# Performance work log

Measured on AMD Instinct MI355X. Metric: run time of the kernel, lower is better.

## Reference

```python
import jax, jax.numpy as jnp
import numpy as np

BS, SEQ, H, L = 2, 4096, 768, 8921

def setup_inputs() -> dict:
    key = jax.random.key(0)
    k1, k2, k3 = jax.random.split(key, 3)
    return {
        "code_features": jax.random.normal(k1, (L, H), dtype=jnp.float32),
        "text_features": jax.random.normal(k2, (BS, SEQ, H), dtype=jnp.float32),
        "attention_mask": jnp.ones((BS, SEQ), dtype=jnp.int32),
        "W": jax.random.normal(k3, (H, H), dtype=jnp.float32) * (1.0 / np.sqrt(H)),
    }

def reference(code_features, text_features, attention_mask, W):
    # projected = tanh(Linear(text)) : (bs, seq, h)
    projected = jnp.tanh(jnp.einsum("bsh,kh->bsk", text_features, W))
    # scores: (bs, seq, labels); code_features broadcasts over batch
    scores = jnp.einsum("bsh,lh->bsl", projected, code_features)
    # softmax over the SEQ axis (dim=1), then transpose -> (bs, labels, seq)
    att_weights = jnp.transpose(jax.nn.softmax(scores, axis=1), (0, 2, 1))
    # weighted sum over seq -> (bs, labels, h)
    weighted_output = jnp.einsum("bls,bsh->blh", att_weights, text_features)
    return (att_weights, weighted_output)
```

## Files before the change

### kernel.cpp

```cpp
#include <hip/hip_runtime.h>
#include <math.h>

#define BSZ  2
#define SEQN 4096
#define HD   768
#define NL   8921

typedef _Float16 f16;
typedef f16   f16x8 __attribute__((ext_vector_type(8)));
typedef float f32x4 __attribute__((ext_vector_type(4)));

#define GPTR(p) ((const __attribute__((address_space(1))) void*)(p))
#define LPTR(p) ((__attribute__((address_space(3))) void*)(p))

__device__ __forceinline__ void stage_region(const f16* __restrict__ src, int ldk,
                                             int row0, int rowMax, int kbase,
                                             f16* region, int t)
{
    const int lane = t & 63, wv = t >> 6;
    #pragma unroll
    for (int qq = 0; qq < 2; ++qq) {
        const int base16 = wv * 64 + qq * 512;
        const int off16  = base16 + lane;
        const int row    = off16 >> 2;
        const int chunk  = off16 & 3;
        const int schunk = chunk ^ ((row >> 1) & 3);
        int grow = row0 + row; if (grow > rowMax) grow = rowMax;
        const f16* g = src + (long long)grow * ldk + kbase + schunk * 8;
        __builtin_amdgcn_global_load_lds(GPTR(g), LPTR(region + base16 * 8), 16, 0, 0);
    }
}

#define PH_SYNC_ENTER()                                          \
    __builtin_amdgcn_sched_barrier(0);                           \
    __builtin_amdgcn_s_barrier();                                \
    asm volatile("s_waitcnt lgkmcnt(0)" ::: "memory");           \
    __builtin_amdgcn_sched_barrier(0);                           \
    __builtin_amdgcn_s_setprio(1);

#define PH_SYNC_EXIT()                                           \
    __builtin_amdgcn_s_setprio(0);                               \
    __builtin_amdgcn_sched_barrier(0);                           \
    __builtin_amdgcn_s_barrier();

template<int OUT>
__global__ __launch_bounds__(512, 2)
void gemm8p(const f16* __restrict__ A, const f16* __restrict__ B,
            void* __restrict__ C, int M, int N, int K,
            long long sA, long long sB, long long sC, int ldA, int ldB)
{
    __shared__ __align__(16) f16 SH[2][2][2][256 * 32];

    const int t    = threadIdx.x;
    const int lane = t & 63;
    const int wv   = t >> 6;
    const int wm   = wv >> 2;
    const int wn   = wv & 3;
    const int rl   = lane & 15;
    const int swz8 = (((lane >> 4) ^ ((rl >> 1) & 3)) * 8);

    const int nx = gridDim.x, nwg = nx * gridDim.y;
    int orig = blockIdx.y * nx + blockIdx.x;
    const int q = nwg >> 3, r = nwg & 7, xcd = orig & 7, sub = orig >> 3;
    const int wg = (xcd < r ? xcd * (q + 1) : r * (q + 1) + (xcd - r) * q) + sub;
    const int bx = wg % nx, by = wg / nx;

    const f16* Ab = A + (long long)blockIdx.z * sA;
    const f16* Bb = B + (long long)blockIdx.z * sB;

    const int m0 = by * 256, n0 = bx * 256;
    const int NT = K >> 6;
    const int Mm1 = M - 1, Nm1 = N - 1;

    f32x4 acc[8][4];
    #pragma unroll
    for (int i = 0; i < 8; ++i)
        #pragma unroll
        for (int j = 0; j < 4; ++j)
            acc[i][j] = (f32x4)0.f;

    stage_region(Ab, ldA, m0, Mm1, 0,  &SH[0][0][0][0], t);
    stage_region(Bb, ldB, n0, Nm1, 0,  &SH[0][1][0][0], t);
    stage_region(Ab, ldA, m0, Mm1, 32, &SH[0][0][1][0], t);
    stage_region(Bb, ldB, n0, Nm1, 32, &SH[0][1][1][0], t);
    stage_region(Ab, ldA, m0, Mm1, 64, &SH[1][0][0][0], t);
    stage_region(Bb, ldB, n0, Nm1, 64, &SH[1][1][0][0], t);
    stage_region(Ab, ldA, m0, Mm1, 96, &SH[1][0][1][0], t);
    asm volatile("s_waitcnt vmcnt(6)" ::: "memory");
    __builtin_amdgcn_sched_barrier(0);
    __builtin_amdgcn_s_barrier();

    for (int tt = 0; tt < NT; ++tt) {
        const int buf = tt & 1;
        const f16* As0 = &SH[buf][0][0][0];
        const f16* As1 = &SH[buf][0][1][0];
        const f16* Bs0 = &SH[buf][1][0][0];
        const f16* Bs1 = &SH[buf][1][1][0];

        f16x8 af[8], bfa, bfb, bfc, bfd;

        #pragma unroll
        for (int f = 0; f < 8; ++f)
            af[f] = *(const f16x8*)&As0[(wm * 128 + f * 16 + rl) * 32 + swz8];
        bfa = *(const f16x8*)&Bs0[(wn * 64 + 0 * 16 + rl) * 32 + swz8];
        bfb = *(const f16x8*)&Bs0[(wn * 64 + 1 * 16 + rl) * 32 + swz8];
        if (tt + 1 < NT)
            stage_region(Bb, ldB, n0, Nm1, (tt + 1) * 64 + 32, &SH[buf ^ 1][1][1][0], t);
        PH_SYNC_ENTER();
        #pragma unroll
        for (int f = 0; f < 8; ++f) {
            acc[f][0] = __builtin_amdgcn_mfma_f32_16x16x32_f16(af[f], bfa, acc[f][0], 0, 0, 0);
            acc[f][1] = __builtin_amdgcn_mfma_f32_16x16x32_f16(af[f], bfb, acc[f][1], 0, 0, 0);
        }
        PH_SYNC_EXIT();

        bfc = *(const f16x8*)&Bs0[(wn * 64 + 2 * 16 + rl) * 32 + swz8];
        bfd = *(const f16x8*)&Bs0[(wn * 64 + 3 * 16 + rl) * 32 + swz8];
        if (tt + 2 < NT)
            stage_region(Ab, ldA, m0, Mm1, (tt + 2) * 64, &SH[buf][0][0][0], t);
        PH_SYNC_ENTER();
        #pragma unroll
        for (int f = 0; f < 8; ++f) {
            acc[f][2] = __builtin_amdgcn_mfma_f32_16x16x32_f16(af[f], bfc, acc[f][2], 0, 0, 0);
            acc[f][3] = __builtin_amdgcn_mfma_f32_16x16x32_f16(af[f], bfd, acc[f][3], 0, 0, 0);
        }
        PH_SYNC_EXIT();

        #pragma unroll
        for (int f = 0; f < 8; ++f)
            af[f] = *(const f16x8*)&As1[(wm * 128 + f * 16 + rl) * 32 + swz8];
        bfa = *(const f16x8*)&Bs1[(wn * 64 + 0 * 16 + rl) * 32 + swz8];
        bfb = *(const f16x8*)&Bs1[(wn * 64 + 1 * 16 + rl) * 32 + swz8];
        if (tt + 2 < NT)
            stage_region(Bb, ldB, n0, Nm1, (tt + 2) * 64, &SH[buf][1][0][0], t);
        PH_SYNC_ENTER();
        #pragma unroll
        for (int f = 0; f < 8; ++f) {
            acc[f][0] = __builtin_amdgcn_mfma_f32_16x16x32_f16(af[f], bfa, acc[f][0], 0, 0, 0);
            acc[f][1] = __builtin_amdgcn_mfma_f32_16x16x32_f16(af[f], bfb, acc[f][1], 0, 0, 0);
        }
        PH_SYNC_EXIT();

        bfc = *(const f16x8*)&Bs1[(wn * 64 + 2 * 16 + rl) * 32 + swz8];
        bfd = *(const f16x8*)&Bs1[(wn * 64 + 3 * 16 + rl) * 32 + swz8];
        if (tt + 2 < NT)
            stage_region(Ab, ldA, m0, Mm1, (tt + 2) * 64 + 32, &SH[buf][0][1][0], t);
        __builtin_amdgcn_sched_barrier(0);
        __builtin_amdgcn_s_barrier();
        asm volatile("s_waitcnt lgkmcnt(0)" ::: "memory");
        __builtin_amdgcn_sched_barrier(0);
        __builtin_amdgcn_s_setprio(1);
        #pragma unroll
        for (int f = 0; f < 8; ++f) {
            acc[f][2] = __builtin_amdgcn_mfma_f32_16x16x32_f16(af[f], bfc, acc[f][2], 0, 0, 0);
            acc[f][3] = __builtin_amdgcn_mfma_f32_16x16x32_f16(af[f], bfd, acc[f][3], 0, 0, 0);
        }
        __builtin_amdgcn_s_setprio(0);
        asm volatile("s_waitcnt vmcnt(6)" ::: "memory");
        __builtin_amdgcn_sched_barrier(0);
        __builtin_amdgcn_s_barrier();
    }

    const int rq = (lane >> 4) * 4;
    #pragma unroll
    for (int f = 0; f < 8; ++f) {
        #pragma unroll
        for (int j = 0; j < 4; ++j) {
            #pragma unroll
            for (int rr = 0; rr < 4; ++rr) {
                const int row = m0 + wm * 128 + f * 16 + rq + rr;
                const int col = n0 + wn * 64 + j * 16 + rl;
                if (row < M) {
                    if constexpr (OUT == 1)
                        ((f16*)C + (long long)blockIdx.z * sC)[(long long)row * N + col] = (f16)acc[f][j][rr];
                    else
                        ((float*)C + (long long)blockIdx.z * sC)[(long long)row * N + col] = acc[f][j][rr];
                }
            }
        }
    }
}

template<int S16>
__device__ inline void stage_tile(const void* srcv, int ldk, int row0, int rowMax,
                                  int kt, f16* dst, int t, int lane, int wv)
{
    if constexpr (S16) {
        const f16* src = (const f16*)srcv;
        #pragma unroll
        for (int j = 0; j < 2; ++j) {
            int r = wv * 32 + j * 16 + (lane >> 2);
            int row = row0 + r; if (row > rowMax) row = rowMax;
            const f16* g = src + (long long)row * ldk + kt + (lane & 3) * 8;
            f16* l = dst + (wv * 32 + j * 16) * 32;
            __builtin_amdgcn_global_load_lds(GPTR(g), LPTR(l), 16, 0, 0);
        }
    } else {
        const float* src = (const float*)srcv;
        int r  = t >> 1;
        int kq = (t & 1) * 16;
        int row = row0 + r; if (row > rowMax) row = rowMax;
        const float* g = src + (long long)row * ldk + kt + kq;
        float4 v0 = ((const float4*)g)[0];
        float4 v1 = ((const float4*)g)[1];
        float4 v2 = ((const float4*)g)[2];
        float4 v3 = ((const float4*)g)[3];
        f16x8 h0, h1;
        h0[0]=(f16)v0.x; h0[1]=(f16)v0.y; h0[2]=(f16)v0.z; h0[3]=(f16)v0.w;
        h0[4]=(f16)v1.x; h0[5]=(f16)v1.y; h0[6]=(f16)v1.z; h0[7]=(f16)v1.w;
        h1[0]=(f16)v2.x; h1[1]=(f16)v2.y; h1[2]=(f16)v2.z; h1[3]=(f16)v2.w;
        h1[4]=(f16)v3.x; h1[5]=(f16)v3.y; h1[6]=(f16)v3.z; h1[7]=(f16)v3.w;
        *(f16x8*)&dst[r * 32 + kq]     = h0;
        *(f16x8*)&dst[r * 32 + kq + 8] = h1;
    }
}

template<int SA, int SB, int OUTMODE>
__global__ __launch_bounds__(256)
void mfma_nt(const void* __restrict__ A, const void* __restrict__ B,
             void* __restrict__ C, int M, int N, int K,
             long long sA, long long sB, long long sC, int ldA, int ldB)
{
    const char* Ab = (const char*)A + (long long)blockIdx.z * sA * (SA ? 2 : 4);
    const char* Bb = (const char*)B + (long long)blockIdx.z * sB * (SB ? 2 : 4);

    __shared__ __align__(16) f16 As[128 * 32];
    __shared__ __align__(16) f16 Bs[128 * 32];

    const int t    = threadIdx.x;
    const int lane = t & 63;
    const int wv   = t >> 6;
    const int wr   = wv >> 1;
    const int wc   = wv & 1;
    const int m0   = blockIdx.y * 128;
    const int n0   = blockIdx.x * 128;

    f32x4 acc[4][4] = {};

    for (int kt = 0; kt < K; kt += 32) {
        stage_tile<SA>(Ab, ldA, m0, M - 1, kt, As, t, lane, wv);
        stage_tile<SB>(Bb, ldB, n0, N - 1, kt, Bs, t, lane, wv);
        __syncthreads();

        f16x8 af[4], bf[4];
        const int kc = (lane >> 4) * 8;
        const int rl = lane & 15;
        #pragma unroll
        for (int i = 0; i < 4; ++i)
            af[i] = *(const f16x8*)&As[(wr * 64 + i * 16 + rl) * 32 + kc];
        #pragma unroll
        for (int j = 0; j < 4; ++j)
            bf[j] = *(const f16x8*)&Bs[(wc * 64 + j * 16 + rl) * 32 + kc];

        #pragma unroll
        for (int i = 0; i < 4; ++i)
            #pragma unroll
            for (int j = 0; j < 4; ++j)
                acc[i][j] = __builtin_amdgcn_mfma_f32_16x16x32_f16(af[i], bf[j], acc[i][j], 0, 0, 0);
        __syncthreads();
    }

    const int rquad = (lane >> 4) * 4;
    const int rcol  = lane & 15;
    #pragma unroll
    for (int i = 0; i < 4; ++i) {
        #pragma unroll
        for (int j = 0; j < 4; ++j) {
            #pragma unroll
            for (int r = 0; r < 4; ++r) {
                int row = m0 + wr * 64 + i * 16 + rquad + r;
                int col = n0 + wc * 64 + j * 16 + rcol;
                if (row < M) {
                    if constexpr (OUTMODE == 1)
                        ((f16*)C)[(long long)row * N + col] = (f16)tanhf(acc[i][j][r]);
                    else
                        ((float*)C + (long long)blockIdx.z * sC)[(long long)row * N + col] = acc[i][j][r];
                }
            }
        }
    }
}

__global__ __launch_bounds__(256)
void cvt_f32_f16(const float* __restrict__ in, f16* __restrict__ out, long long n4)
{
    long long i = (long long)blockIdx.x * 256 + threadIdx.x;
    if (i < n4) {
        float4 v = ((const float4*)in)[i];
        f16 h[4] = {(f16)v.x, (f16)v.y, (f16)v.z, (f16)v.w};
        *(uint2*)&out[i * 4] = *(uint2*)h;
    }
}

__global__ __launch_bounds__(256)
void transpose_f16(const float* __restrict__ in, f16* __restrict__ out)
{
    __shared__ float tile[32][33];
    const int b  = blockIdx.z;
    const int h0 = blockIdx.x * 32, s0 = blockIdx.y * 32;
    in  += (long long)b * SEQN * HD;
    out += (long long)b * HD * SEQN;
    const int tx = threadIdx.x & 31, ty = threadIdx.x >> 5;
    #pragma unroll
    for (int i = ty; i < 32; i += 8)
        tile[i][tx] = in[(long long)(s0 + i) * HD + h0 + tx];
    __syncthreads();
    #pragma unroll
    for (int i = ty; i < 32; i += 8)
        out[(long long)(h0 + i) * SEQN + s0 + tx] = (f16)tile[tx][i];
}

__global__ __launch_bounds__(256)
void softmax_f16(f16* __restrict__ scores, float* __restrict__ att)
{
    const long long row = blockIdx.x;
    f16*   ps = scores + row * (long long)SEQN;
    float* pa = att    + row * (long long)SEQN;
    const int t = threadIdx.x;

    f16x8 h[2];
    float x[2][8];
    float vmax = -INFINITY;
    #pragma unroll
    for (int i = 0; i < 2; ++i) {
        h[i] = ((const f16x8*)ps)[t + 256 * i];
        #pragma unroll
        for (int j = 0; j < 8; ++j) {
            x[i][j] = (float)h[i][j];
            vmax = fmaxf(vmax, x[i][j]);
        }
    }
    #pragma unroll
    for (int off = 32; off > 0; off >>= 1)
        vmax = fmaxf(vmax, __shfl_xor(vmax, off));

    __shared__ float redmax[4];
    __shared__ float redsum[4];
    if ((t & 63) == 0) redmax[t >> 6] = vmax;
    __syncthreads();
    vmax = fmaxf(fmaxf(redmax[0], redmax[1]), fmaxf(redmax[2], redmax[3]));

    float sum = 0.f;
    #pragma unroll
    for (int i = 0; i < 2; ++i)
        #pragma unroll
        for (int j = 0; j < 8; ++j) {
            x[i][j] = expf(x[i][j] - vmax);
            sum += x[i][j];
        }
    #pragma unroll
    for (int off = 32; off > 0; off >>= 1)
        sum += __shfl_xor(sum, off);
    if ((t & 63) == 0) redsum[t >> 6] = sum;
    __syncthreads();
    sum = (redsum[0] + redsum[1]) + (redsum[2] + redsum[3]);

    const float inv = 1.0f / sum;
    #pragma unroll
    for (int i = 0; i < 2; ++i) {
        f16x8 hn;
        #pragma unroll
        for (int j = 0; j < 8; ++j) {
            x[i][j] *= inv;
            hn[j] = (f16)x[i][j];
        }
        float4 lo = make_float4(x[i][0], x[i][1], x[i][2], x[i][3]);
        float4 hi = make_float4(x[i][4], x[i][5], x[i][6], x[i][7]);
        ((float4*)pa)[(t + 256 * i) * 2 + 0] = lo;
        ((float4*)pa)[(t + 256 * i) * 2 + 1] = hi;
        ((f16x8*)ps)[t + 256 * i] = hn;
    }
}

#define BMF 64
#define BNF 64
#define BKF 16
#define PADF 4

__global__ __launch_bounds__(256)
void softmax_rows_f32(float* __restrict__ data)
{
    const long long row = blockIdx.x;
    float* p = data + row * (long long)SEQN;
    const int t = threadIdx.x;
    float4 v[4];
    float vmax = -INFINITY;
    #pragma unroll
    for (int i = 0; i < 4; ++i) {
        v[i] = ((const float4*)p)[t + 256 * i];
        vmax = fmaxf(vmax, fmaxf(fmaxf(v[i].x, v[i].y), fmaxf(v[i].z, v[i].w)));
    }
    #pragma unroll
    for (int off = 32; off > 0; off >>= 1)
        vmax = fmaxf(vmax, __shfl_xor(vmax, off));
    __shared__ float redmax[4];
    __shared__ float redsum[4];
    if ((t & 63) == 0) redmax[t >> 6] = vmax;
    __syncthreads();
    vmax = fmaxf(fmaxf(redmax[0], redmax[1]), fmaxf(redmax[2], redmax[3]));
    float sum = 0.f;
    #pragma unroll
    for (int i = 0; i < 4; ++i) {
        v[i].x = expf(v[i].x - vmax); v[i].y = expf(v[i].y - vmax);
        v[i].z = expf(v[i].z - vmax); v[i].w = expf(v[i].w - vmax);
        sum += (v[i].x + v[i].y) + (v[i].z + v[i].w);
    }
    #pragma unroll
    for (int off = 32; off > 0; off >>= 1)
        sum += __shfl_xor(sum, off);
    if ((t & 63) == 0) redsum[t >> 6] = sum;
    __syncthreads();
    sum = (redsum[0] + redsum[1]) + (redsum[2] + redsum[3]);
    const float inv = 1.0f / sum;
    #pragma unroll
    for (int i = 0; i < 4; ++i) {
        v[i].x *= inv; v[i].y *= inv; v[i].z *= inv; v[i].w *= inv;
        ((float4*)p)[t + 256 * i] = v[i];
    }
}

template<bool TANH>
__global__ __launch_bounds__(256)
void nt_gemm(const float* __restrict__ A, const float* __restrict__ B,
             float* __restrict__ C, int M, int N, int K,
             long long sA, long long sB, long long sC)
{
    A += (long long)blockIdx.z * sA;
    B += (long long)blockIdx.z * sB;
    C += (long long)blockIdx.z * sC;
    __shared__ __align__(16) float As[BKF][BMF + PADF];
    __shared__ __align__(16) float Bs[BKF][BNF + PADF];
    const int t = threadIdx.x;
    const int m0 = blockIdx.y * BMF, n0 = blockIdx.x * BNF;
    const int tx = t & 15, ty = t >> 4, lr = t >> 2, lk = (t & 3) * 4;
    float acc[4][4] = {};
    for (int kt = 0; kt < K; kt += BKF) {
        {
            float4 v = make_float4(0.f, 0.f, 0.f, 0.f);
            int m = m0 + lr;
            if (m < M) v = *(const float4*)(A + (long long)m * K + kt + lk);
            As[lk+0][lr]=v.x; As[lk+1][lr]=v.y; As[lk+2][lr]=v.z; As[lk+3][lr]=v.w;
        }
        {
            float4 v = make_float4(0.f, 0.f, 0.f, 0.f);
            int n = n0 + lr;
            if (n < N) v = *(const float4*)(B + (long long)n * K + kt + lk);
            Bs[lk+0][lr]=v.x; Bs[lk+1][lr]=v.y; Bs[lk+2][lr]=v.z; Bs[lk+3][lr]=v.w;
        }
        __syncthreads();
        #pragma unroll
        for (int k = 0; k < BKF; ++k) {
            float4 a = *(const float4*)(&As[k][ty * 4]);
            float4 b = *(const float4*)(&Bs[k][tx * 4]);
            float av[4]={a.x,a.y,a.z,a.w}, bv[4]={b.x,b.y,b.z,b.w};
            #pragma unroll
            for (int i = 0; i < 4; ++i)
                #pragma unroll
                for (int j = 0; j < 4; ++j)
                    acc[i][j] = fmaf(av[i], bv[j], acc[i][j]);
        }
        __syncthreads();
    }
    #pragma unroll
    for (int i = 0; i < 4; ++i) {
        int m = m0 + ty * 4 + i;
        if (m < M) {
            float4 r;
            r.x = TANH ? tanhf(acc[i][0]) : acc[i][0];
            r.y = TANH ? tanhf(acc[i][1]) : acc[i][1];
            r.z = TANH ? tanhf(acc[i][2]) : acc[i][2];
            r.w = TANH ? tanhf(acc[i][3]) : acc[i][3];
            *(float4*)(C + (long long)m * N + n0 + tx * 4) = r;
        }
    }
}

__global__ __launch_bounds__(256)
void nn_gemm(const float* __restrict__ A, const float* __restrict__ B,
             float* __restrict__ C, int M, int N, int K,
             long long sA, long long sB, long long sC)
{
    A += (long long)blockIdx.z * sA;
    B += (long long)blockIdx.z * sB;
    C += (long long)blockIdx.z * sC;
    __shared__ __align__(16) float As[BKF][BMF + PADF];
    __shared__ __align__(16) float Bs[BKF][BNF + PADF];
    const int t = threadIdx.x;
    const int m0 = blockIdx.y * BMF, n0 = blockIdx.x * BNF;
    const int tx = t & 15, ty = t >> 4, lr = t >> 2, lk = (t & 3) * 4;
    const int kr = t >> 4, cq = (t & 15) * 4;
    float acc[4][4] = {};
    for (int kt = 0; kt < K; kt += BKF) {
        {
            float4 v = make_float4(0.f, 0.f, 0.f, 0.f);
            int m = m0 + lr;
            if (m < M) v = *(const float4*)(A + (long long)m * K + kt + lk);
            As[lk+0][lr]=v.x; As[lk+1][lr]=v.y; As[lk+2][lr]=v.z; As[lk+3][lr]=v.w;
        }
        {
            float4 v = *(const float4*)(B + (long long)(kt + kr) * N + n0 + cq);
            *(float4*)(&Bs[kr][cq]) = v;
        }
        __syncthreads();
        #pragma unroll
        for (int k = 0; k < BKF; ++k) {
            float4 a = *(const float4*)(&As[k][ty * 4]);
            float4 b = *(const float4*)(&Bs[k][tx * 4]);
            float av[4]={a.x,a.y,a.z,a.w}, bv[4]={b.x,b.y,b.z,b.w};
            #pragma unroll
            for (int i = 0; i < 4; ++i)
                #pragma unroll
                for (int j = 0; j < 4; ++j)
                    acc[i][j] = fmaf(av[i], bv[j], acc[i][j]);
        }
        __syncthreads();
    }
    #pragma unroll
    for (int i = 0; i < 4; ++i) {
        int m = m0 + ty * 4 + i;
        if (m < M)
            *(float4*)(C + (long long)m * N + n0 + tx * 4) =
                make_float4(acc[i][0], acc[i][1], acc[i][2], acc[i][3]);
    }
}

extern "C" void kernel_launch(void* const* d_in, const int* in_sizes, int n_in,
                              void* d_out, int out_size, void* d_ws, size_t ws_size,
                              hipStream_t stream)
{
    const float* code = (const float*)d_in[0];
    const float* text = (const float*)d_in[1];
    const float* Wm   = (const float*)d_in[3];

    float* att  = (float*)d_out;
    float* wout = att + (long long)BSZ * NL * SEQN;

    const long long n_code  = (long long)NL * HD;
    const long long n_proj  = (long long)BSZ * SEQN * HD;
    const long long n_textT = (long long)BSZ * HD * SEQN;
    const long long n_att   = (long long)BSZ * NL * SEQN;
    const size_t need_bytes = (size_t)(n_code + n_proj + n_textT + n_att) * 2;

    if (ws_size < need_bytes) {
        float* proj = wout;
        dim3 g1(HD / BNF, (BSZ * SEQN) / BMF, 1);
        hipLaunchKernelGGL((nt_gemm<true>), g1, dim3(256), 0, stream,
                           text, Wm, proj, BSZ * SEQN, HD, HD, 0LL, 0LL, 0LL);
        dim3 g2(SEQN / BNF, (NL + BMF - 1) / BMF, BSZ);
        hipLaunchKernelGGL((nt_gemm<false>), g2, dim3(256), 0, stream,
                           code, proj, att, NL, SEQN, HD,
                           0LL, (long long)SEQN * HD, (long long)NL * SEQN);
        hipLaunchKernelGGL(softmax_rows_f32, dim3(BSZ * NL), dim3(256), 0, stream, att);
        dim3 g4(HD / BNF, (NL + BMF - 1) / BMF, BSZ);
        hipLaunchKernelGGL(nn_gemm, g4, dim3(256), 0, stream,
                           att, text, wout, NL, HD, SEQN,
                           (long long)NL * SEQN, (long long)SEQN * HD, (long long)NL * HD);
        return;
    }

    f16* code_h   = (f16*)d_ws;
    f16* proj_h   = code_h + n_code;
    f16* textT_h  = proj_h + n_proj;
    f16* scores_h = textT_h + n_textT;

    {
        long long n4 = n_code / 4;
        hipLaunchKernelGGL(cvt_f32_f16, dim3((unsigned)((n4 + 255) / 256)), dim3(256), 0, stream,
                           code, code_h, n4);
    }
    {
        dim3 g(HD / 32, SEQN / 32, BSZ);
        hipLaunchKernelGGL(transpose_f16, g, dim3(256), 0, stream, text, textT_h);
    }
    {
        dim3 g(HD / 128, (BSZ * SEQN) / 128, 1);
        hipLaunchKernelGGL((mfma_nt<0, 0, 1>), g, dim3(256), 0, stream,
                           text, Wm, proj_h, BSZ * SEQN, HD, HD, 0LL, 0LL, 0LL, HD, HD);
    }
    {
        dim3 g(SEQN / 256, (NL + 255) / 256, BSZ);
        hipLaunchKernelGGL((gemm8p<1>), g, dim3(512), 0, stream,
                           code_h, proj_h, scores_h, NL, SEQN, HD,
                           0LL, (long long)SEQN * HD, (long long)NL * SEQN, HD, HD);
    }
    hipLaunchKernelGGL(softmax_f16, dim3(BSZ * NL), dim3(256), 0, stream, scores_h, att);
    {
        dim3 g(HD / 256, (NL + 255) / 256, BSZ);
        hipLaunchKernelGGL((gemm8p<0>), g, dim3(512), 0, stream,
                           scores_h, textT_h, wout, NL, HD, SEQN,
                           (long long)NL * SEQN, (long long)HD * SEQN, (long long)NL * HD,
                           SEQN, SEQN);
    }
}
```

Before: 419.6 us.

## Fuse fp32 attention-weight writeback into the weighted-sum GEMM's LDS pipeline

```diff
diff --git a/kernel.cpp b/kernel.cpp
--- a/kernel.cpp
+++ b/kernel.cpp
@@ -43,11 +43,12 @@
     __builtin_amdgcn_sched_barrier(0);                           \
     __builtin_amdgcn_s_barrier();
 
-template<int OUT>
+template<int OUT, int WB>
 __global__ __launch_bounds__(512, 2)
 void gemm8p(const f16* __restrict__ A, const f16* __restrict__ B,
             void* __restrict__ C, int M, int N, int K,
-            long long sA, long long sB, long long sC, int ldA, int ldB)
+            long long sA, long long sB, long long sC, int ldA, int ldB,
+            float* __restrict__ attO)
 {
     __shared__ __align__(16) f16 SH[2][2][2][256 * 32];
 
@@ -71,6 +72,17 @@
     const int m0 = by * 256, n0 = bx * 256;
     const int NT = K >> 6;
     const int Mm1 = M - 1, Nm1 = N - 1;
+
+    const int wb_lo = WB ? (bx * NT) / nx : 0;
+    const int wb_hi = WB ? ((bx + 1) * NT) / nx : 0;
+    const int rb_slot = t * 2;
+    const int rb_row  = rb_slot >> 2;
+    const int rb_cp0  = rb_slot & 3;
+    const int rb_x    = (rb_row >> 1) & 3;
+    float* attRow = nullptr;
+    if constexpr (WB) {
+        attRow = attO + (long long)blockIdx.z * sA + (long long)(m0 + rb_row) * ldA;
+    }
 
     f32x4 acc[8][4];
     #pragma unroll
@@ -97,13 +109,19 @@
         const f16* Bs0 = &SH[buf][1][0][0];
         const f16* Bs1 = &SH[buf][1][1][0];
 
+        const bool wb = WB && (tt >= wb_lo) && (tt < wb_hi);
         f16x8 af[8], bfa, bfb, bfc, bfd;
+        f16x8 rb0, rb1;
 
         #pragma unroll
         for (int f = 0; f < 8; ++f)
             af[f] = *(const f16x8*)&As0[(wm * 128 + f * 16 + rl) * 32 + swz8];
         bfa = *(const f16x8*)&Bs0[(wn * 64 + 0 * 16 + rl) * 32 + swz8];
         bfb = *(const f16x8*)&Bs0[(wn * 64 + 1 * 16 + rl) * 32 + swz8];
+        if (wb) {
+            rb0 = *(const f16x8*)&As0[rb_slot * 8];
+            rb1 = *(const f16x8*)&As0[(rb_slot + 1) * 8];
+        }
         if (tt + 1 < NT)
             stage_region(Bb, ldB, n0, Nm1, (tt + 1) * 64 + 32, &SH[buf ^ 1][1][1][0], t);
         PH_SYNC_ENTER();
@@ -112,7 +130,22 @@
             acc[f][0] = __builtin_amdgcn_mfma_f32_16x16x32_f16(af[f], bfa, acc[f][0], 0, 0, 0);
             acc[f][1] = __builtin_amdgcn_mfma_f32_16x16x32_f16(af[f], bfb, acc[f][1], 0, 0, 0);
         }
-        PH_SYNC_EXIT();
+        __builtin_amdgcn_s_setprio(0);
+        if (wb && m0 + rb_row < M) {
+            float* d = attRow + tt * 64;
+            const int c0 = rb_cp0 ^ rb_x, c1 = (rb_cp0 + 1) ^ rb_x;
+            float4 v;
+            v = make_float4((float)rb0[0], (float)rb0[1], (float)rb0[2], (float)rb0[3]);
+            *(float4*)(d + c0 * 8)     = v;
+            v = make_float4((float)rb0[4], (float)rb0[5], (float)rb0[6], (float)rb0[7]);
+            *(float4*)(d + c0 * 8 + 4) = v;
+            v = make_float4((float)rb1[0], (float)rb1[1], (float)rb1[2], (float)rb1[3]);
+            *(float4*)(d + c1 * 8)     = v;
+            v = make_float4((float)rb1[4], (float)rb1[5], (float)rb1[6], (float)rb1[7]);
+            *(float4*)(d + c1 * 8 + 4) = v;
+        }
+        __builtin_amdgcn_sched_barrier(0);
+        __builtin_amdgcn_s_barrier();
 
         bfc = *(const f16x8*)&Bs0[(wn * 64 + 2 * 16 + rl) * 32 + swz8];
         bfd = *(const f16x8*)&Bs0[(wn * 64 + 3 * 16 + rl) * 32 + swz8];
@@ -131,6 +164,10 @@
             af[f] = *(const f16x8*)&As1[(wm * 128 + f * 16 + rl) * 32 + swz8];
         bfa = *(const f16x8*)&Bs1[(wn * 64 + 0 * 16 + rl) * 32 + swz8];
         bfb = *(const f16x8*)&Bs1[(wn * 64 + 1 * 16 + rl) * 32 + swz8];
+        if (wb) {
+            rb0 = *(const f16x8*)&As1[rb_slot * 8];
+            rb1 = *(const f16x8*)&As1[(rb_slot + 1) * 8];
+        }
         if (tt + 2 < NT)
             stage_region(Bb, ldB, n0, Nm1, (tt + 2) * 64, &SH[buf][1][0][0], t);
         PH_SYNC_ENTER();
@@ -139,7 +176,22 @@
             acc[f][0] = __builtin_amdgcn_mfma_f32_16x16x32_f16(af[f], bfa, acc[f][0], 0, 0, 0);
             acc[f][1] = __builtin_amdgcn_mfma_f32_16x16x32_f16(af[f], bfb, acc[f][1], 0, 0, 0);
         }
-        PH_SYNC_EXIT();
+        __builtin_amdgcn_s_setprio(0);
+        if (wb && m0 + rb_row < M) {
+            float* d = attRow + tt * 64 + 32;
+            const int c0 = rb_cp0 ^ rb_x, c1 = (rb_cp0 + 1) ^ rb_x;
+            float4 v;
+            v = make_float4((float)rb0[0], (float)rb0[1], (float)rb0[2], (float)rb0[3]);
+            *(float4*)(d + c0 * 8)     = v;
+            v = make_float4((float)rb0[4], (float)rb0[5], (float)rb0[6], (float)rb0[7]);
+            *(float4*)(d + c0 * 8 + 4) = v;
+            v = make_float4((float)rb1[0], (float)rb1[1], (float)rb1[2], (float)rb1[3]);
+            *(float4*)(d + c1 * 8)     = v;
+            v = make_float4((float)rb1[4], (float)rb1[5], (float)rb1[6], (float)rb1[7]);
+            *(float4*)(d + c1 * 8 + 4) = v;
+        }
+        __builtin_amdgcn_sched_barrier(0);
+        __builtin_amdgcn_s_barrier();
 
         bfc = *(const f16x8*)&Bs1[(wn * 64 + 2 * 16 + rl) * 32 + swz8];
         bfd = *(const f16x8*)&Bs1[(wn * 64 + 3 * 16 + rl) * 32 + swz8];
@@ -311,11 +363,10 @@
 }
 
 __global__ __launch_bounds__(256)
-void softmax_f16(f16* __restrict__ scores, float* __restrict__ att)
+void softmax_f16(f16* __restrict__ scores)
 {
     const long long row = blockIdx.x;
-    f16*   ps = scores + row * (long long)SEQN;
-    float* pa = att    + row * (long long)SEQN;
+    f16* ps = scores + row * (long long)SEQN;
     const int t = threadIdx.x;
 
     f16x8 h[2];
@@ -360,14 +411,8 @@
     for (int i = 0; i < 2; ++i) {
         f16x8 hn;
         #pragma unroll
-        for (int j = 0; j < 8; ++j) {
-            x[i][j] *= inv;
-            hn[j] = (f16)x[i][j];
-        }
-        float4 lo = make_float4(x[i][0], x[i][1], x[i][2], x[i][3]);
-        float4 hi = make_float4(x[i][4], x[i][5], x[i][6], x[i][7]);
-        ((float4*)pa)[(t + 256 * i) * 2 + 0] = lo;
-        ((float4*)pa)[(t + 256 * i) * 2 + 1] = hi;
+        for (int j = 0; j < 8; ++j)
+            hn[j] = (f16)(x[i][j] * inv);
         ((f16x8*)ps)[t + 256 * i] = hn;
     }
 }
@@ -579,16 +624,17 @@
     }
     {
         dim3 g(SEQN / 256, (NL + 255) / 256, BSZ);
-        hipLaunchKernelGGL((gemm8p<1>), g, dim3(512), 0, stream,
+        hipLaunchKernelGGL((gemm8p<1, 0>), g, dim3(512), 0, stream,
                            code_h, proj_h, scores_h, NL, SEQN, HD,
-                           0LL, (long long)SEQN * HD, (long long)NL * SEQN, HD, HD);
-    }
-    hipLaunchKernelGGL(softmax_f16, dim3(BSZ * NL), dim3(256), 0, stream, scores_h, att);
+                           0LL, (long long)SEQN * HD, (long long)NL * SEQN, HD, HD,
+                           (float*)nullptr);
+    }
+    hipLaunchKernelGGL(softmax_f16, dim3(BSZ * NL), dim3(256), 0, stream, scores_h);
     {
         dim3 g(HD / 256, (NL + 255) / 256, BSZ);
-        hipLaunchKernelGGL((gemm8p<0>), g, dim3(512), 0, stream,
+        hipLaunchKernelGGL((gemm8p<0, 1>), g, dim3(512), 0, stream,
                            scores_h, textT_h, wout, NL, HD, SEQN,
                            (long long)NL * SEQN, (long long)HD * SEQN, (long long)NL * HD,
-                           SEQN, SEQN);
-    }
-}
+                           SEQN, SEQN, att);
+    }
+}
```

Result: slower. 460.3 us (+9.7%).
